# Kernel tuning notes

Hardware: AMD Instinct MI355X
Metric: run time of the kernel (lower is better)

Reference implementation:

```python
import jax, jax.numpy as jnp
import numpy as np

N_HEAD = 16
D_HEAD = 64
D_MODEL = 1024
N_ROLL = 3
SCALE = 1.0 / (D_HEAD ** 0.5)
EPS = 1e-5


def mul_roll_repeat(x, n_roll):
    # concat of x * roll(x, i) over i=1..n_roll along last dim
    return jnp.concatenate([x * jnp.roll(x, i, axis=-1) for i in range(1, n_roll + 1)], axis=-1)


def dpfp(x):
    # DPFP feature map: [relu(x), relu(-x)] then roll-multiply-repeat
    x2 = jnp.concatenate([jax.nn.relu(x), jax.nn.relu(-x)], axis=-1)
    return mul_roll_repeat(x2, N_ROLL)


def layer_norm(x, gamma, beta):
    mu = jnp.mean(x, axis=-1, keepdims=True)
    var = jnp.var(x, axis=-1, keepdims=True)
    return (x - mu) * jax.lax.rsqrt(var + 1e-5) * gamma + beta


def setup_inputs() -> dict:
    key = jax.random.key(0)
    ks = jax.random.split(key, 4)
    S, B = 2048, 2
    h = jax.random.normal(ks[0], (S, B, D_MODEL), dtype=jnp.float32)
    Wq = jax.random.normal(ks[1], (D_MODEL, N_HEAD * D_HEAD), dtype=jnp.float32) * 0.02
    Wkv = jax.random.normal(ks[2], (D_MODEL, 2 * N_HEAD * D_HEAD), dtype=jnp.float32) * 0.02
    Wo = jax.random.normal(ks[3], (N_HEAD * D_HEAD, D_MODEL), dtype=jnp.float32) * 0.02
    ln_gamma = jnp.ones((D_MODEL,), dtype=jnp.float32)
    ln_beta = jnp.zeros((D_MODEL,), dtype=jnp.float32)
    return {"h": h, "Wq": Wq, "Wkv": Wkv, "Wo": Wo, "ln_gamma": ln_gamma, "ln_beta": ln_beta}


def reference(h, Wq, Wkv, Wo, ln_gamma, ln_beta):
    # h: [S, B, D_MODEL]; mems=None, attn_mask=None, post-LN, eval (no dropout)
    S, B, _ = h.shape
    q = (h @ Wq).reshape(S, B, N_HEAD, D_HEAD)
    kv = h @ Wkv
    k, v = jnp.split(kv, 2, axis=-1)
    k = k.reshape(S, B, N_HEAD, D_HEAD)
    v = v.reshape(S, B, N_HEAD, D_HEAD)

    pq = dpfp(q)  # [S, B, N, F], F = 2*D_HEAD*N_ROLL = 384
    pk = dpfp(k)

    # Linear-attention form: identical math to the original quadratic
    # einsum('ibnd,jbnd->ijbn') * scale, summed over j for the denominator,
    # since there is no mask and dropatt=0. Avoids the O(S^2) score tensor.
    kv_agg = jnp.einsum('jbnf,jbnd->bnfd', pk, v)          # [B, N, F, D]
    z = pk.sum(axis=0)                                      # [B, N, F]
    num = jnp.einsum('ibnf,bnfd->ibnd', pq, kv_agg) * SCALE  # [S, B, N, D]
    den = jnp.einsum('ibnf,bnf->ibn', pq, z) * SCALE + EPS   # [S, B, N]
    attn_vec = (num / den[..., None]).reshape(S, B, N_HEAD * D_HEAD)

    attn_out = attn_vec @ Wo
    return layer_norm(h + attn_out, ln_gamma, ln_beta)
```

## Files before the change

### kernel.cpp

```cpp
#include <hip/hip_runtime.h>
#include <math.h>

#define NH 16
#define DM 1024
#define FEAT 384
#define SB 4096
#define SEQ 2048

static constexpr float SCALE = 0.125f;
static constexpr float EPS = 1e-5f;

typedef __attribute__((ext_vector_type(8))) _Float16 half8;
typedef __attribute__((ext_vector_type(4))) _Float16 half4;
typedef __attribute__((ext_vector_type(4))) float f32x4;

#define AS1 __attribute__((address_space(1)))
#define AS3 __attribute__((address_space(3)))

#define IDX(r, o) ((((r) << 6)) + ((((o) ^ ((r) & 7))) << 3))

__global__ __launch_bounds__(256) void prep_kernel(const float* __restrict__ h,
                                                   const float* __restrict__ Wq,
                                                   const float* __restrict__ Wkv,
                                                   const float* __restrict__ Wo,
                                                   _Float16* __restrict__ h_h,
                                                   _Float16* __restrict__ WqkvT,
                                                   _Float16* __restrict__ WoT) {
    __shared__ _Float16 tile[32][33];
    int bid = blockIdx.x, t = threadIdx.x;
    if (bid < 4096) {
        int i = bid * 256 + t;
        const float4 v = ((const float4*)h)[i];
        half4 o = {(_Float16)v.x, (_Float16)v.y, (_Float16)v.z, (_Float16)v.w};
        ((half4*)h_h)[i] = o;
        return;
    }
    const float* src;
    _Float16* dst;
    int N, col0, n0, k0;
    if (bid < 7168) {
        int b2 = bid - 4096;
        n0 = (b2 % 96) * 32; k0 = (b2 / 96) * 32;
        if (n0 < 1024) { src = Wq; N = 1024; col0 = n0; }
        else           { src = Wkv; N = 2048; col0 = n0 - 1024; }
        dst = WqkvT;
    } else {
        int b3 = bid - 7168;
        n0 = (b3 & 31) * 32; k0 = (b3 >> 5) * 32;
        src = Wo; N = 1024; col0 = n0; dst = WoT;
    }
    int tx = t & 31, ty = t >> 5;
    #pragma unroll
    for (int i = 0; i < 4; ++i)
        tile[ty + i * 8][tx] = (_Float16)src[(size_t)(k0 + ty + i * 8) * N + col0 + tx];
    __syncthreads();
    #pragma unroll
    for (int i = 0; i < 4; ++i)
        dst[(size_t)(n0 + ty + i * 8) * 1024 + k0 + tx] = tile[tx][ty + i * 8];
}

template <int MH, int NB>
__device__ __forceinline__ void mfma_quad(f32x4 (&acc)[8][4], half8 (&a)[4][2],
                                          half8 (&bv)[4][2]) {
    #pragma unroll
    for (int mf = 0; mf < 4; ++mf)
        #pragma unroll
        for (int nf = 0; nf < 2; ++nf)
            #pragma unroll
            for (int ks = 0; ks < 2; ++ks)
                acc[MH * 4 + mf][NB * 2 + nf] = __builtin_amdgcn_mfma_f32_16x16x32_f16(
                    a[mf][ks], bv[NB * 2 + nf][ks], acc[MH * 4 + mf][NB * 2 + nf], 0, 0, 0);
}

__global__ __launch_bounds__(512) void gemm_f16_8ph(const _Float16* __restrict__ A,
                                                    const _Float16* __restrict__ BT,
                                                    _Float16* __restrict__ C,
                                                    int M, int N, int K) {
    __shared__ _Float16 smem[65536];
    const int t = threadIdx.x;
    const int w = t >> 6, l = t & 63;
    const int wr = w >> 2, wc = w & 3;
    const int NT = K >> 6;
    const int NHT = K >> 4;

    int nwg = gridDim.x;
    int cpx = nwg >> 3;
    int bid = blockIdx.x;
    int swz = (bid & 7) * cpx + (bid >> 3);
    int ntile = N >> 8;
    int row0 = (swz / ntile) << 8;
    int col0 = (swz % ntile) << 8;

    f32x4 acc[8][4];
    #pragma unroll
    for (int m = 0; m < 8; ++m)
        #pragma unroll
        for (int n = 0; n < 4; ++n)
            acc[m][n] = (f32x4){0.f, 0.f, 0.f, 0.f};

    const int lr = l >> 3;
    const int lc8 = ((l & 7) ^ lr) * 8;

    auto STAGE = [&](int s) {
        if (s >= NHT) return;
        int tau = s >> 2, hh = s & 3;
        int kk = tau << 6;
        int hf = hh & 1;
        int ldsbase = ((tau & 1) << 15) + ((hh >= 2) ? 0 : 16384) + (hf << 13)
                    + ((w * 2) << 9);
        const _Float16* gbase = (hh >= 2)
            ? A + (size_t)(row0 + hf * 128) * K
            : BT + (size_t)(col0 + hf * 128) * K;
        #pragma unroll
        for (int i = 0; i < 2; ++i) {
            const _Float16* src = gbase + (size_t)((w * 2 + i) * 8 + lr) * K + kk + lc8;
            __builtin_amdgcn_global_load_lds((const AS1 void*)src,
                                             (AS3 void*)(smem + ldsbase + (i << 9)), 16, 0, 0);
        }
    };

    half8 a[4][2], bv[4][2];
    auto LDA = [&](int mh, int bufb) {
        #pragma unroll
        for (int mf = 0; mf < 4; ++mf) {
            int r = wr * 128 + (mh * 4 + mf) * 16 + (l & 15);
            #pragma unroll
            for (int ks = 0; ks < 2; ++ks) {
                int c16 = (ks * 4 + (l >> 4)) ^ (r & 7);
                a[mf][ks] = *(const half8*)&smem[bufb + r * 64 + c16 * 8];
            }
        }
    };
    auto LDB = [&](int bufb) {
        #pragma unroll
        for (int nf = 0; nf < 4; ++nf) {
            int r = wc * 64 + nf * 16 + (l & 15);
            #pragma unroll
            for (int ks = 0; ks < 2; ++ks) {
                int c16 = (ks * 4 + (l >> 4)) ^ (r & 7);
                bv[nf][ks] = *(const half8*)&smem[bufb + 16384 + r * 64 + c16 * 8];
            }
        }
    };

    #pragma unroll 1
    for (int s = 0; s < 7; ++s) STAGE(s);
    asm volatile("s_waitcnt vmcnt(6)" ::: "memory");
    __builtin_amdgcn_s_barrier();

    #pragma unroll 1
    for (int ti = 0; ti < NT; ++ti) {
        const int bufb = (ti & 1) << 15;
        const int sb = 7 + (ti << 2);
        LDA(0, bufb); LDB(bufb);
        STAGE(sb);
        __builtin_amdgcn_sched_barrier(0);
        __builtin_amdgcn_s_barrier();
        asm volatile("s_waitcnt lgkmcnt(0)" ::: "memory");
        __builtin_amdgcn_sched_barrier(0);
        __builtin_amdgcn_s_setprio(1);
        mfma_quad<0, 0>(acc, a, bv);
        __builtin_amdgcn_s_setprio(0);
        __builtin_amdgcn_sched_barrier(0);
        __builtin_amdgcn_s_barrier();
        STAGE(sb + 1);
        __builtin_amdgcn_sched_barrier(0);
        __builtin_amdgcn_s_barrier();
        __builtin_amdgcn_s_setprio(1);
        mfma_quad<0, 1>(acc, a, bv);
        __builtin_amdgcn_s_setprio(0);
        __builtin_amdgcn_sched_barrier(0);
        __builtin_amdgcn_s_barrier();
        LDA(1, bufb);
        STAGE(sb + 2);
        __builtin_amdgcn_sched_barrier(0);
        __builtin_amdgcn_s_barrier();
        asm volatile("s_waitcnt lgkmcnt(0)" ::: "memory");
        __builtin_amdgcn_sched_barrier(0);
        __builtin_amdgcn_s_setprio(1);
        mfma_quad<1, 0>(acc, a, bv);
        __builtin_amdgcn_s_setprio(0);
        __builtin_amdgcn_sched_barrier(0);
        __builtin_amdgcn_s_barrier();
        STAGE(sb + 3);
        __builtin_amdgcn_sched_barrier(0);
        __builtin_amdgcn_s_barrier();
        __builtin_amdgcn_s_setprio(1);
        mfma_quad<1, 1>(acc, a, bv);
        __builtin_amdgcn_s_setprio(0);
        __builtin_amdgcn_sched_barrier(0);
        if (ti < NT - 2) asm volatile("s_waitcnt vmcnt(6)" ::: "memory");
        else             asm volatile("s_waitcnt vmcnt(0)" ::: "memory");
        __builtin_amdgcn_s_barrier();
    }

    int ocol = l & 15, orow4 = (l >> 4) * 4;
    #pragma unroll
    for (int mf = 0; mf < 8; ++mf)
        #pragma unroll
        for (int nf = 0; nf < 4; ++nf) {
            size_t base = (size_t)(row0 + wr * 128 + mf * 16 + orow4) * N
                        + col0 + wc * 64 + nf * 16 + ocol;
            #pragma unroll
            for (int j = 0; j < 4; ++j)
                C[base + (size_t)j * N] = (_Float16)acc[mf][nf][j];
        }
}

__global__ __launch_bounds__(256) void gemm_f16(const _Float16* __restrict__ A,
                                                const _Float16* __restrict__ BT,
                                                _Float16* __restrict__ C,
                                                int M, int N, int K) {
    __shared__ _Float16 Asb[128 * 32];
    __shared__ _Float16 Bsb[128 * 32];
    int t = threadIdx.x;
    int w = t >> 6, l = t & 63;
    int wr = w >> 1, wc = w & 1;
    int row0 = blockIdx.y * 128, col0 = blockIdx.x * 128;

    f32x4 acc[4][4];
    #pragma unroll
    for (int m = 0; m < 4; ++m)
        #pragma unroll
        for (int n = 0; n < 4; ++n)
            acc[m][n] = (f32x4){0.f, 0.f, 0.f, 0.f};

    int srow = l >> 2;
    int scol = (l & 3) * 8;

    for (int k0 = 0; k0 < K; k0 += 32) {
        #pragma unroll
        for (int i = 0; i < 2; ++i) {
            int chunk = w * 2 + i;
            const _Float16* asrc =
                A + (size_t)(row0 + chunk * 16 + srow) * K + k0 + scol;
            __builtin_amdgcn_global_load_lds((const AS1 void*)asrc,
                                             (AS3 void*)(Asb + chunk * 512), 16, 0, 0);
            const _Float16* bsrc =
                BT + (size_t)(col0 + chunk * 16 + srow) * K + k0 + scol;
            __builtin_amdgcn_global_load_lds((const AS1 void*)bsrc,
                                             (AS3 void*)(Bsb + chunk * 512), 16, 0, 0);
        }
        __syncthreads();
        int rsel = l & 15, csel = (l >> 4) * 8;
        half8 a[4], b[4];
        #pragma unroll
        for (int m = 0; m < 4; ++m)
            a[m] = *(const half8*)&Asb[(wr * 64 + m * 16 + rsel) * 32 + csel];
        #pragma unroll
        for (int n = 0; n < 4; ++n)
            b[n] = *(const half8*)&Bsb[(wc * 64 + n * 16 + rsel) * 32 + csel];
        #pragma unroll
        for (int m = 0; m < 4; ++m)
            #pragma unroll
            for (int n = 0; n < 4; ++n)
                acc[m][n] = __builtin_amdgcn_mfma_f32_16x16x32_f16(a[m], b[n], acc[m][n], 0, 0, 0);
        __syncthreads();
    }

    int ocol = l & 15, orow = (l >> 4) * 4;
    #pragma unroll
    for (int m = 0; m < 4; ++m)
        #pragma unroll
        for (int n = 0; n < 4; ++n) {
            size_t base = (size_t)(row0 + wr * 64 + m * 16 + orow) * N
                        + col0 + wc * 64 + n * 16 + ocol;
            #pragma unroll
            for (int j = 0; j < 4; ++j)
                C[base + (size_t)j * N] = (_Float16)acc[m][n][j];
        }
}

__global__ __launch_bounds__(512) void kvagg_fused(const _Float16* __restrict__ qkv,
                                                   float* __restrict__ kvp,
                                                   float* __restrict__ zp) {
    __shared__ _Float16 x2s[128 * 64];
    __shared__ _Float16 vTs[64 * 64];
    __shared__ _Float16 pkTs[384 * 64];
    const int t = threadIdx.x;
    const int w = t >> 6, l = t & 63;
    const int bn = blockIdx.x;
    const int jseg = blockIdx.y;
    const int b = bn >> 4, nh = bn & 15;

    f32x4 acc[4][3];
    #pragma unroll
    for (int mf = 0; mf < 4; ++mf)
        #pragma unroll
        for (int nf = 0; nf < 3; ++nf)
            acc[mf][nf] = (f32x4){0.f, 0.f, 0.f, 0.f};
    float zacc[3] = {0.f, 0.f, 0.f};

    const int sc = t & 63;
    const int so = t >> 6;

    #pragma unroll 1
    for (int ch = 0; ch < 4; ++ch) {
        int j0 = jseg * 256 + ch * 64;
        _Float16 kx[8], vx[8];
        #pragma unroll
        for (int e = 0; e < 8; ++e) {
            size_t rb = (size_t)((j0 + so * 8 + e) * 2 + b) * 3072 + nh * 64 + sc;
            kx[e] = qkv[rb + 1024];
            vx[e] = qkv[rb + 2048];
        }
        half8 xlo, xhi, vv;
        #pragma unroll
        for (int e = 0; e < 8; ++e) {
            float kf = (float)kx[e];
            xlo[e] = (_Float16)fmaxf(kf, 0.f);
            xhi[e] = (_Float16)fmaxf(-kf, 0.f);
            vv[e] = vx[e];
        }
        if (ch) __syncthreads();
        *(half8*)&x2s[IDX(sc, so)] = xlo;
        *(half8*)&x2s[IDX(sc + 64, so)] = xhi;
        *(half8*)&vTs[IDX(sc, so)] = vv;
        __syncthreads();
        {
            const int o = t & 7;
            const int fb = t >> 3;
            #pragma unroll
            for (int it = 0; it < 6; ++it) {
                int f = it * 64 + fb;
                int fm = f & 127;
                int r = (f >> 7) + 1;
                int fm2 = (fm - r) & 127;
                half8 pa = *(const half8*)&x2s[IDX(fm, o)];
                half8 pb = *(const half8*)&x2s[IDX(fm2, o)];
                *(half8*)&pkTs[IDX(f, o)] = pa * pb;
            }
        }
        __syncthreads();
        #pragma unroll
        for (int ks = 0; ks < 2; ++ks) {
            half8 a[4], bq[3];
            int oo = ks * 4 + (l >> 4);
            #pragma unroll
            for (int mf = 0; mf < 4; ++mf) {
                int dr = mf * 16 + (l & 15);
                a[mf] = *(const half8*)&vTs[IDX(dr, oo)];
            }
            #pragma unroll
            for (int nf = 0; nf < 3; ++nf) {
                int fr = w * 48 + nf * 16 + (l & 15);
                bq[nf] = *(const half8*)&pkTs[IDX(fr, oo)];
                #pragma unroll
                for (int e = 0; e < 8; ++e) zacc[nf] += (float)bq[nf][e];
            }
            #pragma unroll
            for (int mf = 0; mf < 4; ++mf)
                #pragma unroll
                for (int nf = 0; nf < 3; ++nf)
                    acc[mf][nf] = __builtin_amdgcn_mfma_f32_16x16x32_f16(
                        a[mf], bq[nf], acc[mf][nf], 0, 0, 0);
        }
    }

    #pragma unroll
    for (int nf = 0; nf < 3; ++nf) {
        float v = zacc[nf];
        v += __shfl_xor(v, 16, 64);
        v += __shfl_xor(v, 32, 64);
        if (l < 16)
            zp[(size_t)(jseg * 32 + bn) * FEAT + w * 48 + nf * 16 + l] = v;
    }
    float* outp = kvp + (size_t)(jseg * 32 + bn) * 64 * FEAT;
    int orow = (l >> 4) * 4, ocol = l & 15;
    #pragma unroll
    for (int mf = 0; mf < 4; ++mf)
        #pragma unroll
        for (int nf = 0; nf < 3; ++nf) {
            int fcol = w * 48 + nf * 16 + ocol;
            #pragma unroll
            for (int j = 0; j < 4; ++j)
                outp[(size_t)(mf * 16 + orow + j) * FEAT + fcol] = acc[mf][nf][j];
        }
}

__global__ __launch_bounds__(256) void reduceA(const float* __restrict__ kvp,
                                               const float* __restrict__ zp,
                                               _Float16* __restrict__ kvaggT,
                                               float* __restrict__ z) {
    const int NKV = 32 * 64 * FEAT;
    int idx = blockIdx.x * 256 + threadIdx.x;
    if (idx < NKV) {
        float s = 0.f;
        #pragma unroll
        for (int c = 0; c < 8; ++c) s += kvp[(size_t)c * NKV + idx];
        kvaggT[idx] = (_Float16)s;
    } else if (idx < NKV + 32 * FEAT) {
        int e = idx - NKV;
        float s = 0.f;
        #pragma unroll
        for (int c = 0; c < 8; ++c) s += zp[c * 32 * FEAT + e];
        z[e] = s;
    }
}

template <int F0>
__device__ __forceinline__ void pq_half(const float (&qr)[64], _Float16* prow) {
    #pragma unroll
    for (int g8 = 0; g8 < 24; ++g8) {
        half8 o;
        #pragma unroll
        for (int e = 0; e < 8; ++e) {
            const int f = F0 + g8 * 8 + e;
            const int fm = f & 127;
            const int r = (f >> 7) + 1;
            const int fm2 = (fm - r) & 127;
            float a = (fm < 64) ? fmaxf(qr[fm], 0.f) : fmaxf(-qr[fm - 64], 0.f);
            float bb = (fm2 < 64) ? fmaxf(qr[fm2], 0.f) : fmaxf(-qr[fm2 - 64], 0.f);
            o[e] = (_Float16)(a * bb);
        }
        *(half8*)&prow[F0 + g8 * 8] = o;
    }
}

#define PQ_STR 392
__global__ __launch_bounds__(256) void attn_fused(const _Float16* __restrict__ qkv,
                                                  const _Float16* __restrict__ kvaggT,
                                                  const float* __restrict__ z,
                                                  _Float16* __restrict__ av) {
    __shared__ _Float16 pq_lds[128 * PQ_STR];
    __shared__ _Float16 B_lds[64 * PQ_STR];
    __shared__ float z_lds[FEAT];
    __shared__ float den_lds[128];
    int t = threadIdx.x;
    int w = t >> 6, l = t & 63;
    int iblk = blockIdx.x;
    int bn = blockIdx.y;
    int b = bn >> 4, nh = bn & 15;

    {
        const _Float16* Bg = kvaggT + (size_t)bn * 64 * FEAT;
        #pragma unroll
        for (int s = 0; s < 12; ++s) {
            int idx8 = t + 256 * s;
            half8 vv = *(const half8*)&Bg[idx8 * 8];
            int row = idx8 / 48, col8 = idx8 - row * 48;
            *(half8*)&B_lds[row * PQ_STR + col8 * 8] = vv;
        }
    }
    for (int e = t; e < FEAT; e += 256) z_lds[e] = z[(size_t)bn * FEAT + e];

    {
        int il = t & 127;
        int ig = iblk * 128 + il;
        const _Float16* qrow = qkv + ((size_t)ig * 2 + b) * 3072 + nh * 64;
        float qr[64];
        #pragma unroll
        for (int e2 = 0; e2 < 8; ++e2) {
            half8 vv = *(const half8*)&qrow[e2 * 8];
            #pragma unroll
            for (int e = 0; e < 8; ++e) qr[e2 * 8 + e] = (float)vv[e];
        }
        _Float16* prow = &pq_lds[il * PQ_STR];
        if (t < 128) pq_half<0>(qr, prow);
        else         pq_half<192>(qr, prow);
    }
    __syncthreads();

    f32x4 acc[2][4];
    #pragma unroll
    for (int m = 0; m < 2; ++m)
        #pragma unroll
        for (int n = 0; n < 4; ++n)
            acc[m][n] = (f32x4){0.f, 0.f, 0.f, 0.f};
    float denacc[2] = {0.f, 0.f};
    int rsel = l & 15, csel = (l >> 4) * 8;

    #pragma unroll
    for (int k0 = 0; k0 < FEAT; k0 += 32) {
        half8 a[2], bfr[4];
        #pragma unroll
        for (int m = 0; m < 2; ++m)
            a[m] = *(const half8*)&pq_lds[(w * 32 + m * 16 + rsel) * PQ_STR + k0 + csel];
        #pragma unroll
        for (int n = 0; n < 4; ++n)
            bfr[n] = *(const half8*)&B_lds[(n * 16 + rsel) * PQ_STR + k0 + csel];
        #pragma unroll
        for (int m = 0; m < 2; ++m)
            #pragma unroll
            for (int e = 0; e < 8; ++e)
                denacc[m] += (float)a[m][e] * z_lds[k0 + csel + e];
        #pragma unroll
        for (int m = 0; m < 2; ++m)
            #pragma unroll
            for (int n = 0; n < 4; ++n)
                acc[m][n] = __builtin_amdgcn_mfma_f32_16x16x32_f16(a[m], bfr[n], acc[m][n], 0, 0, 0);
    }

    #pragma unroll
    for (int m = 0; m < 2; ++m) {
        float v = denacc[m];
        v += __shfl_xor(v, 16, 64);
        v += __shfl_xor(v, 32, 64);
        if (l < 16) den_lds[w * 32 + m * 16 + l] = v;
    }
    __syncthreads();

    int orow = (l >> 4) * 4, ocol = l & 15;
    #pragma unroll
    for (int m = 0; m < 2; ++m)
        #pragma unroll
        for (int n = 0; n < 4; ++n)
            #pragma unroll
            for (int j = 0; j < 4; ++j) {
                int row = w * 32 + m * 16 + orow + j;
                float den = den_lds[row] * SCALE + EPS;
                float val = acc[m][n][j] * SCALE / den;
                int i = iblk * 128 + row;
                av[((size_t)i * 2 + b) * 1024 + nh * 64 + n * 16 + ocol] = (_Float16)val;
            }
}

__global__ __launch_bounds__(256) void ln_kernel(const float* __restrict__ h,
                                                 const _Float16* __restrict__ attn_out,
                                                 const float* __restrict__ gamma,
                                                 const float* __restrict__ beta,
                                                 float* __restrict__ out) {
    int r = blockIdx.x;
    int t = threadIdx.x;
    const float4 hv = ((const float4*)(h + (size_t)r * 1024))[t];
    const half4 a4 = ((const half4*)(attn_out + (size_t)r * 1024))[t];
    float x[4] = {hv.x + (float)a4[0], hv.y + (float)a4[1],
                  hv.z + (float)a4[2], hv.w + (float)a4[3]};
    float sum = x[0] + x[1] + x[2] + x[3];
    float sq = x[0]*x[0] + x[1]*x[1] + x[2]*x[2] + x[3]*x[3];
    #pragma unroll
    for (int off = 32; off >= 1; off >>= 1) {
        sum += __shfl_xor(sum, off, 64);
        sq += __shfl_xor(sq, off, 64);
    }
    __shared__ float ssum[4], ssq[4];
    int wl = t >> 6, lane = t & 63;
    if (lane == 0) { ssum[wl] = sum; ssq[wl] = sq; }
    __syncthreads();
    sum = ssum[0] + ssum[1] + ssum[2] + ssum[3];
    sq = ssq[0] + ssq[1] + ssq[2] + ssq[3];
    float mu = sum * (1.f / 1024.f);
    float var = sq * (1.f / 1024.f) - mu * mu;
    float rs = rsqrtf(var + 1e-5f);
    const float4 g4 = ((const float4*)gamma)[t];
    const float4 b4 = ((const float4*)beta)[t];
    float4 o;
    o.x = (x[0] - mu) * rs * g4.x + b4.x;
    o.y = (x[1] - mu) * rs * g4.y + b4.y;
    o.z = (x[2] - mu) * rs * g4.z + b4.z;
    o.w = (x[3] - mu) * rs * g4.w + b4.w;
    ((float4*)(out + (size_t)r * 1024))[t] = o;
}

extern "C" void kernel_launch(void* const* d_in, const int* in_sizes, int n_in,
                              void* d_out, int out_size, void* d_ws, size_t ws_size,
                              hipStream_t stream) {
    const float* h     = (const float*)d_in[0];
    const float* Wq    = (const float*)d_in[1];
    const float* Wkv   = (const float*)d_in[2];
    const float* Wo    = (const float*)d_in[3];
    const float* gamma = (const float*)d_in[4];
    const float* beta  = (const float*)d_in[5];
    float* out = (float*)d_out;
    _Float16* u = (_Float16*)d_ws;

    _Float16* h_h    = u;
    _Float16* WqkvT  = u + 4194304;
    _Float16* WoT    = u + 7340032;
    _Float16* qkv    = u + 8388608;
    float*    kvp    = (float*)(u + 20971520);
    float*    zp     = (float*)(u + 33554432);
    _Float16* kvaggT = u + 33751040;
    float*    z      = (float*)(u + 34537472);
    _Float16* av         = h_h;
    _Float16* attn_out_h = qkv;

    dim3 blk(256);
    prep_kernel<<<dim3(8192), blk, 0, stream>>>(h, Wq, Wkv, Wo, h_h, WqkvT, WoT);
    gemm_f16_8ph<<<dim3(192), dim3(512), 0, stream>>>(h_h, WqkvT, qkv, SB, 3072, DM);
    kvagg_fused<<<dim3(32, 8), dim3(512), 0, stream>>>(qkv, kvp, zp);
    reduceA<<<dim3(3120), blk, 0, stream>>>(kvp, zp, kvaggT, z);
    attn_fused<<<dim3(16, 32), blk, 0, stream>>>(qkv, kvaggT, z, av);
    gemm_f16<<<dim3(8, 32), blk, 0, stream>>>(av, WoT, attn_out_h, SB, 1024, DM);
    ln_kernel<<<dim3(SB), blk, 0, stream>>>(h, attn_out_h, gamma, beta, out);
}
```

Baseline: 116.9 us.

## Retile QKV GEMM to 256x192 tiles so the grid fills all CUs

New measurement: 111.6 us. 4.5% less time.

```diff
diff --git a/kernel.cpp b/kernel.cpp
--- a/kernel.cpp
+++ b/kernel.cpp
@@ -59,107 +59,129 @@
         dst[(size_t)(n0 + ty + i * 8) * 1024 + k0 + tx] = tile[tx][ty + i * 8];
 }
 
-template <int MH, int NB>
-__device__ __forceinline__ void mfma_quad(f32x4 (&acc)[8][4], half8 (&a)[4][2],
-                                          half8 (&bv)[4][2]) {
+template <int MH>
+__device__ __forceinline__ void mfma_n01(f32x4 (&acc)[8][3], half8 (&a)[4][2],
+                                         half8 (&bv)[3][2]) {
     #pragma unroll
     for (int mf = 0; mf < 4; ++mf)
         #pragma unroll
         for (int nf = 0; nf < 2; ++nf)
             #pragma unroll
             for (int ks = 0; ks < 2; ++ks)
-                acc[MH * 4 + mf][NB * 2 + nf] = __builtin_amdgcn_mfma_f32_16x16x32_f16(
-                    a[mf][ks], bv[NB * 2 + nf][ks], acc[MH * 4 + mf][NB * 2 + nf], 0, 0, 0);
+                acc[MH * 4 + mf][nf] = __builtin_amdgcn_mfma_f32_16x16x32_f16(
+                    a[mf][ks], bv[nf][ks], acc[MH * 4 + mf][nf], 0, 0, 0);
+}
+template <int MH>
+__device__ __forceinline__ void mfma_n2(f32x4 (&acc)[8][3], half8 (&a)[4][2],
+                                        half8 (&bv)[3][2]) {
+    #pragma unroll
+    for (int mf = 0; mf < 4; ++mf)
+        #pragma unroll
+        for (int ks = 0; ks < 2; ++ks)
+            acc[MH * 4 + mf][2] = __builtin_amdgcn_mfma_f32_16x16x32_f16(
+                a[mf][ks], bv[2][ks], acc[MH * 4 + mf][2], 0, 0, 0);
 }
 
 __global__ __launch_bounds__(512) void gemm_f16_8ph(const _Float16* __restrict__ A,
                                                     const _Float16* __restrict__ BT,
                                                     _Float16* __restrict__ C,
                                                     int M, int N, int K) {
-    __shared__ _Float16 smem[65536];
+    __shared__ _Float16 smem[57344];
     const int t = threadIdx.x;
     const int w = t >> 6, l = t & 63;
     const int wr = w >> 2, wc = w & 3;
     const int NT = K >> 6;
-    const int NHT = K >> 4;
+    const int NU = K >> 4;
 
     int nwg = gridDim.x;
     int cpx = nwg >> 3;
     int bid = blockIdx.x;
     int swz = (bid & 7) * cpx + (bid >> 3);
-    int ntile = N >> 8;
+    int ntile = N / 192;
     int row0 = (swz / ntile) << 8;
-    int col0 = (swz % ntile) << 8;
-
-    f32x4 acc[8][4];
+    int col0 = (swz % ntile) * 192;
+
+    f32x4 acc[8][3];
     #pragma unroll
     for (int m = 0; m < 8; ++m)
         #pragma unroll
-        for (int n = 0; n < 4; ++n)
+        for (int n = 0; n < 3; ++n)
             acc[m][n] = (f32x4){0.f, 0.f, 0.f, 0.f};
 
     const int lr = l >> 3;
     const int lc8 = ((l & 7) ^ lr) * 8;
 
     auto STAGE = [&](int s) {
-        if (s >= NHT) return;
-        int tau = s >> 2, hh = s & 3;
+        if (s >= NU) return;
+        int tau = s >> 2, u = s & 3;
         int kk = tau << 6;
-        int hf = hh & 1;
-        int ldsbase = ((tau & 1) << 15) + ((hh >= 2) ? 0 : 16384) + (hf << 13)
-                    + ((w * 2) << 9);
-        const _Float16* gbase = (hh >= 2)
-            ? A + (size_t)(row0 + hf * 128) * K
-            : BT + (size_t)(col0 + hf * 128) * K;
-        #pragma unroll
-        for (int i = 0; i < 2; ++i) {
-            const _Float16* src = gbase + (size_t)((w * 2 + i) * 8 + lr) * K + kk + lc8;
+        int bufo = (tau & 1) * 28672;
+        if (u == 0) {
+            #pragma unroll
+            for (int i = 0; i < 2; ++i) {
+                int chunk = w * 2 + i;
+                const _Float16* src = BT + (size_t)(col0 + chunk * 8 + lr) * K + kk + lc8;
+                __builtin_amdgcn_global_load_lds((const AS1 void*)src,
+                    (AS3 void*)(smem + bufo + 16384 + chunk * 512), 16, 0, 0);
+            }
+        } else if (u == 1) {
+            const _Float16* src = BT + (size_t)(col0 + 128 + w * 8 + lr) * K + kk + lc8;
             __builtin_amdgcn_global_load_lds((const AS1 void*)src,
-                                             (AS3 void*)(smem + ldsbase + (i << 9)), 16, 0, 0);
+                (AS3 void*)(smem + bufo + 24576 + w * 512), 16, 0, 0);
+        } else {
+            int rbase = (u == 3) ? 128 : 0;
+            int lbase = (u == 3) ? 8192 : 0;
+            #pragma unroll
+            for (int i = 0; i < 2; ++i) {
+                int chunk = w * 2 + i;
+                const _Float16* src = A + (size_t)(row0 + rbase + chunk * 8 + lr) * K + kk + lc8;
+                __builtin_amdgcn_global_load_lds((const AS1 void*)src,
+                    (AS3 void*)(smem + bufo + lbase + chunk * 512), 16, 0, 0);
+            }
         }
     };
 
-    half8 a[4][2], bv[4][2];
-    auto LDA = [&](int mh, int bufb) {
+    half8 a[4][2], bv[3][2];
+    auto LDA = [&](int mh, int bufo) {
         #pragma unroll
         for (int mf = 0; mf < 4; ++mf) {
             int r = wr * 128 + (mh * 4 + mf) * 16 + (l & 15);
             #pragma unroll
             for (int ks = 0; ks < 2; ++ks) {
                 int c16 = (ks * 4 + (l >> 4)) ^ (r & 7);
-                a[mf][ks] = *(const half8*)&smem[bufb + r * 64 + c16 * 8];
+                a[mf][ks] = *(const half8*)&smem[bufo + r * 64 + c16 * 8];
             }
         }
     };
-    auto LDB = [&](int bufb) {
-        #pragma unroll
-        for (int nf = 0; nf < 4; ++nf) {
-            int r = wc * 64 + nf * 16 + (l & 15);
+    auto LDB = [&](int bufo) {
+        #pragma unroll
+        for (int nf = 0; nf < 3; ++nf) {
+            int r = wc * 48 + nf * 16 + (l & 15);
             #pragma unroll
             for (int ks = 0; ks < 2; ++ks) {
                 int c16 = (ks * 4 + (l >> 4)) ^ (r & 7);
-                bv[nf][ks] = *(const half8*)&smem[bufb + 16384 + r * 64 + c16 * 8];
+                bv[nf][ks] = *(const half8*)&smem[bufo + 16384 + r * 64 + c16 * 8];
             }
         }
     };
 
     #pragma unroll 1
     for (int s = 0; s < 7; ++s) STAGE(s);
-    asm volatile("s_waitcnt vmcnt(6)" ::: "memory");
+    asm volatile("s_waitcnt vmcnt(5)" ::: "memory");
     __builtin_amdgcn_s_barrier();
 
     #pragma unroll 1
     for (int ti = 0; ti < NT; ++ti) {
-        const int bufb = (ti & 1) << 15;
+        const int bufo = (ti & 1) * 28672;
         const int sb = 7 + (ti << 2);
-        LDA(0, bufb); LDB(bufb);
+        LDA(0, bufo); LDB(bufo);
         STAGE(sb);
         __builtin_amdgcn_sched_barrier(0);
         __builtin_amdgcn_s_barrier();
         asm volatile("s_waitcnt lgkmcnt(0)" ::: "memory");
         __builtin_amdgcn_sched_barrier(0);
         __builtin_amdgcn_s_setprio(1);
-        mfma_quad<0, 0>(acc, a, bv);
+        mfma_n01<0>(acc, a, bv);
         __builtin_amdgcn_s_setprio(0);
         __builtin_amdgcn_sched_barrier(0);
         __builtin_amdgcn_s_barrier();
@@ -167,18 +189,18 @@
         __builtin_amdgcn_sched_barrier(0);
         __builtin_amdgcn_s_barrier();
         __builtin_amdgcn_s_setprio(1);
-        mfma_quad<0, 1>(acc, a, bv);
+        mfma_n2<0>(acc, a, bv);
         __builtin_amdgcn_s_setprio(0);
         __builtin_amdgcn_sched_barrier(0);
         __builtin_amdgcn_s_barrier();
-        LDA(1, bufb);
+        LDA(1, bufo);
         STAGE(sb + 2);
         __builtin_amdgcn_sched_barrier(0);
         __builtin_amdgcn_s_barrier();
         asm volatile("s_waitcnt lgkmcnt(0)" ::: "memory");
         __builtin_amdgcn_sched_barrier(0);
         __builtin_amdgcn_s_setprio(1);
-        mfma_quad<1, 0>(acc, a, bv);
+        mfma_n01<1>(acc, a, bv);
         __builtin_amdgcn_s_setprio(0);
         __builtin_amdgcn_sched_barrier(0);
         __builtin_amdgcn_s_barrier();
@@ -186,10 +208,10 @@
         __builtin_amdgcn_sched_barrier(0);
         __builtin_amdgcn_s_barrier();
         __builtin_amdgcn_s_setprio(1);
-        mfma_quad<1, 1>(acc, a, bv);
+        mfma_n2<1>(acc, a, bv);
         __builtin_amdgcn_s_setprio(0);
         __builtin_amdgcn_sched_barrier(0);
-        if (ti < NT - 2) asm volatile("s_waitcnt vmcnt(6)" ::: "memory");
+        if (ti < NT - 2) asm volatile("s_waitcnt vmcnt(5)" ::: "memory");
         else             asm volatile("s_waitcnt vmcnt(0)" ::: "memory");
         __builtin_amdgcn_s_barrier();
     }
@@ -198,9 +220,9 @@
     #pragma unroll
     for (int mf = 0; mf < 8; ++mf)
         #pragma unroll
-        for (int nf = 0; nf < 4; ++nf) {
+        for (int nf = 0; nf < 3; ++nf) {
             size_t base = (size_t)(row0 + wr * 128 + mf * 16 + orow4) * N
-                        + col0 + wc * 64 + nf * 16 + ocol;
+                        + col0 + wc * 48 + nf * 16 + ocol;
             #pragma unroll
             for (int j = 0; j < 4; ++j)
                 C[base + (size_t)j * N] = (_Float16)acc[mf][nf][j];
@@ -577,7 +599,7 @@
 
     dim3 blk(256);
     prep_kernel<<<dim3(8192), blk, 0, stream>>>(h, Wq, Wkv, Wo, h_h, WqkvT, WoT);
-    gemm_f16_8ph<<<dim3(192), dim3(512), 0, stream>>>(h_h, WqkvT, qkv, SB, 3072, DM);
+    gemm_f16_8ph<<<dim3(256), dim3(512), 0, stream>>>(h_h, WqkvT, qkv, SB, 3072, DM);
     kvagg_fused<<<dim3(32, 8), dim3(512), 0, stream>>>(qkv, kvp, zp);
     reduceA<<<dim3(3120), blk, 0, stream>>>(kvp, zp, kvaggT, z);
     attn_fused<<<dim3(16, 32), blk, 0, stream>>>(qkv, kvaggT, z, av);
```
